# Performance work log

Hardware: AMD Instinct MI355X
Metric: run time of the kernel (lower is better)

## Reference

```python
import jax, jax.numpy as jnp
import numpy as np

INVALID = 1e9  # distance value marking a missing arc (>= 1e6 threshold in source)
TEMPERATURE = 0.5


def setup_inputs() -> dict:
    n = 4096
    key = jax.random.key(0)
    k_d, k_m, k_l = jax.random.split(key, 3)
    dist = jax.random.uniform(k_d, (n, n), dtype=jnp.float32, minval=0.0, maxval=100.0)
    keep = jax.random.uniform(k_m, (n, n)) < 0.5
    distance_matrix = jnp.where(keep, dist, INVALID).astype(jnp.float32)
    logits = (-2.0 + 0.5 * jax.random.normal(k_l, (n, n))).astype(jnp.float32)
    attention_logits = jnp.zeros((n, n), dtype=jnp.float32)
    return {
        "distance_matrix": distance_matrix,
        "logits": logits,
        "attention_logits": attention_logits,
        "source": 0,
        "destination": n - 1,
    }


def reference(distance_matrix, logits, attention_logits, source, destination):
    n = distance_matrix.shape[0]
    valid = (distance_matrix < 1e6).astype(jnp.float32)
    density = jnp.sum(valid) / (n * n)
    mu1 = 1.0
    mu2 = 10.0 * (1.0 + density)
    mu3 = 10.0 * (1.0 + density)

    # decision matrix (dense branch)
    attention = jax.nn.softmax(attention_logits, axis=1)
    x = jax.nn.sigmoid(logits / TEMPERATURE) * attention * valid  # [n, n]

    # flow penalty: vectorized form of the per-node loop
    out_flow = jnp.sum(x, axis=1)  # [n]
    in_flow = jnp.sum(x, axis=0)   # [n]
    d = out_flow - in_flow
    d = d.at[source].add(-1.0).at[destination].add(1.0)
    flow_penalty = jnp.sum(d * d)

    path_cost = jnp.sum(distance_matrix * x)  # invalid arcs have x == 0
    binary_penalty = jnp.sum(x * (1.0 - x))

    # connectivity: 10-step matmul power iteration (min(n-1, 10) = 10 for n > 11)
    reach = x
    for _ in range(10):
        reach = jnp.minimum(reach + reach @ x, 1.0)
    connectivity_penalty = jnp.square(1.0 - reach[source, destination])

    sparsity_penalty = jnp.sum(x) / (n * n)
    n_edges = jnp.sum(valid)

    return (mu1 * path_cost / (n_edges + 1e-6)
            + mu2 * flow_penalty / n
            + mu3 * binary_penalty / (n * n)
            + 20.0 * connectivity_penalty
            + 5.0 * sparsity_penalty)
```

## Files before the change

### kernel.cpp

```cpp
#include <hip/hip_runtime.h>
#include <hip/hip_bf16.h>
#include <cmath>

typedef unsigned short u16;
typedef unsigned int u32;

__device__ __forceinline__ float bf2f(u16 b) {
    return __uint_as_float(((u32)b) << 16);
}
__device__ __forceinline__ u16 f2bf(float f) {
    u32 u = __float_as_uint(f);
    u = (u + 0x7fffu + ((u >> 16) & 1u)) >> 16;
    return (u16)u;
}

__device__ __forceinline__ float wave_sum(float v) {
#pragma unroll
    for (int o = 32; o > 0; o >>= 1) v += __shfl_xor(v, o, 64);
    return v;
}

__device__ float block_sum(float v) {
    __shared__ float s[4];
    v = wave_sum(v);
    __syncthreads();
    if ((threadIdx.x & 63) == 0) s[threadIdx.x >> 6] = v;
    __syncthreads();
    return s[0] + s[1] + s[2] + s[3];
}

template <int NF4>
__global__ __launch_bounds__(256, 2) void k_main(
    const float* __restrict__ dist, const float* __restrict__ logit,
    const float* __restrict__ attn, const int* __restrict__ srcp,
    u16* __restrict__ xb, float* __restrict__ out_flow,
    float* __restrict__ cnt_row, float* __restrict__ s2_row,
    float* __restrict__ pc_row, float* __restrict__ v, int n) {
    const int lane = threadIdx.x & 63;
    const int wv = threadIdx.x >> 6;
    const int row = blockIdx.x * 4 + wv;
    const size_t base = (size_t)row * n;

    u32 apk[2 * NF4];
    float se = 0.f;
#pragma unroll
    for (int k = 0; k < NF4; ++k) {
        const float4 a = *(const float4*)(attn + base + 4 * lane + 256 * k);
        const float e0 = __expf(a.x), e1 = __expf(a.y);
        const float e2 = __expf(a.z), e3 = __expf(a.w);
        se += (e0 + e1) + (e2 + e3);
        apk[2 * k]     = ((u32)f2bf(e1) << 16) | (u32)f2bf(e0);
        apk[2 * k + 1] = ((u32)f2bf(e3) << 16) | (u32)f2bf(e2);
    }
    const float invZ = 1.0f / wave_sum(se);
    const int src = *srcp;

    float cnt = 0.f, s1 = 0.f, s2 = 0.f, pc = 0.f;
#pragma unroll
    for (int k = 0; k < NF4; ++k) {
        const int col = 4 * lane + 256 * k;
        const float4 df = *(const float4*)(dist + base + col);
        const float4 lf = *(const float4*)(logit + base + col);
        const float dv[4] = {df.x, df.y, df.z, df.w};
        const float lv[4] = {lf.x, lf.y, lf.z, lf.w};
        const float av[4] = {bf2f((u16)(apk[2 * k] & 0xffffu)),
                             bf2f((u16)(apk[2 * k] >> 16)),
                             bf2f((u16)(apk[2 * k + 1] & 0xffffu)),
                             bf2f((u16)(apk[2 * k + 1] >> 16))};
        float xv[4];
        ushort4 pk;
        u16* pkp = (u16*)&pk;
#pragma unroll
        for (int q = 0; q < 4; ++q) {
            float valid = (dv[q] < 1.0e6f) ? 1.f : 0.f;
            float sg = 1.0f / (1.0f + __expf(-2.0f * lv[q]));
            float x = sg * (av[q] * invZ) * valid;
            xv[q] = x;
            cnt += valid;
            s1 += x;
            s2 += x * x;
            pc += dv[q] * x;
            pkp[q] = f2bf(x);
        }
        *(ushort4*)(xb + base + col) = pk;
        if (row == src) {
            float4 vf; vf.x = xv[0]; vf.y = xv[1]; vf.z = xv[2]; vf.w = xv[3];
            *(float4*)(v + col) = vf;
        }
    }
#pragma unroll
    for (int o = 32; o > 0; o >>= 1) {
        cnt += __shfl_xor(cnt, o, 64);
        s1  += __shfl_xor(s1, o, 64);
        s2  += __shfl_xor(s2, o, 64);
        pc  += __shfl_xor(pc, o, 64);
    }
    if (lane == 0) {
        out_flow[row] = s1;
        cnt_row[row] = cnt;
        s2_row[row] = s2;
        pc_row[row] = pc;
    }
}

template <int FIRST>
__global__ __launch_bounds__(256) void k_iter(
    const u16* __restrict__ xb, const float* __restrict__ v_in,
    const float* __restrict__ up_in, float* __restrict__ v_out,
    float* __restrict__ up_out, float* __restrict__ ip,
    int n, int nbx, int rc) {
    __shared__ float vl[64];
    __shared__ float vparts[4][64];
    const int t = threadIdx.x;
    const int lin = blockIdx.x;
    const int xcd = lin & 7;
    const int slot = lin >> 3;
    const int bx = slot % nbx;
    const int by = xcd * ((gridDim.x >> 3) / nbx) + slot / nbx;
    const int rows_per = n / rc;
    const int i0 = by * rows_per;
    const int j0 = bx * 1024 + t * 4;

    if (FIRST) {
        if (t < rows_per) {
            float a = v_in[i0 + t];
            vl[t] = a;
            if (bx == 0) v_out[i0 + t] = a;
        }
    } else {
        const int i = t & 63, g = t >> 6;
        const int cpg = rc >> 2;
        float a = 0.f;
#pragma unroll 4
        for (int c = g * cpg; c < (g + 1) * cpg; ++c)
            a += up_in[(size_t)c * n + i0 + i];
        vparts[g][i] = a;
        __syncthreads();
        if (t < rows_per) {
            float s = v_in[i0 + t] + vparts[0][t] + vparts[1][t] +
                      vparts[2][t] + vparts[3][t];
            vl[t] = s;
            if (bx == 0) v_out[i0 + t] = s;
        }
    }
    __syncthreads();

    float4 acc = {0.f, 0.f, 0.f, 0.f};
    float4 cs = {0.f, 0.f, 0.f, 0.f};
#pragma unroll 8
    for (int i = 0; i < rows_per; ++i) {
        ushort4 xv = *(const ushort4*)(xb + (size_t)(i0 + i) * n + j0);
        float vi = vl[i];
        acc.x = fmaf(vi, bf2f(xv.x), acc.x);
        acc.y = fmaf(vi, bf2f(xv.y), acc.y);
        acc.z = fmaf(vi, bf2f(xv.z), acc.z);
        acc.w = fmaf(vi, bf2f(xv.w), acc.w);
        if (FIRST) {
            cs.x += bf2f(xv.x); cs.y += bf2f(xv.y);
            cs.z += bf2f(xv.z); cs.w += bf2f(xv.w);
        }
    }
    *(float4*)(up_out + (size_t)by * n + j0) = acc;
    if (FIRST) *(float4*)(ip + (size_t)by * n + j0) = cs;
}

__global__ __launch_bounds__(256) void k_reduce(
    const float* __restrict__ out_flow, const float* __restrict__ ip,
    const float* __restrict__ cnt_row, const float* __restrict__ s2_row,
    const float* __restrict__ pc_row, const int* __restrict__ srcp,
    const int* __restrict__ dstp, float* __restrict__ pb, int n, int nchunk) {
    const int t = threadIdx.x;
    const int j = blockIdx.x * 256 + t;
    const int src = *srcp, dst = *dstp;
    float infl = 0.f;
#pragma unroll 8
    for (int c = 0; c < nchunk; ++c) infl += ip[(size_t)c * n + j];
    float d = out_flow[j] - infl;
    if (j == src) d -= 1.f;
    if (j == dst) d += 1.f;
    float f = block_sum(d * d);
    float s1 = block_sum(out_flow[j]);
    float cnt = block_sum(cnt_row[j]);
    float s2 = block_sum(s2_row[j]);
    float pc = block_sum(pc_row[j]);
    if (t == 0) {
        float* p = pb + blockIdx.x * 5;
        p[0] = f; p[1] = s1; p[2] = cnt; p[3] = s2; p[4] = pc;
    }
}

__global__ __launch_bounds__(256) void k_final(
    const float* __restrict__ pb, const float* __restrict__ v_last,
    const float* __restrict__ up_last, const int* __restrict__ dstp,
    float* __restrict__ out, int n, int nblk, int nchunk) {
    const int t = threadIdx.x;
    const int dst = *dstp;
    float flow = block_sum(t < nblk ? pb[t * 5 + 0] : 0.f);
    float S1   = block_sum(t < nblk ? pb[t * 5 + 1] : 0.f);
    float NE   = block_sum(t < nblk ? pb[t * 5 + 2] : 0.f);
    float S2   = block_sum(t < nblk ? pb[t * 5 + 3] : 0.f);
    float PC   = block_sum(t < nblk ? pb[t * 5 + 4] : 0.f);
    float r = block_sum(t < nchunk ? up_last[(size_t)t * n + dst] : 0.f);
    if (t == 0) {
        r += v_last[dst];
        float nf = (float)n;
        float nn = nf * nf;
        float density = NE / nn;
        float mu2 = 10.f * (1.f + density);
        float om = 1.f - r;
        float res = PC / (NE + 1e-6f)
                  + mu2 * flow / nf
                  + mu2 * (S1 - S2) / nn
                  + 20.f * om * om
                  + 5.f * S1 / nn;
        out[0] = res;
    }
}

extern "C" void kernel_launch(void* const* d_in, const int* in_sizes, int n_in,
                              void* d_out, int out_size, void* d_ws, size_t ws_size,
                              hipStream_t stream) {
    const float* dist = (const float*)d_in[0];
    const float* logit = (const float*)d_in[1];
    const float* attn = (const float*)d_in[2];
    const int* srcp = (const int*)d_in[3];
    const int* dstp = (const int*)d_in[4];
    const int n = (int)(std::sqrt((double)in_sizes[0]) + 0.5);
    const size_t nn = (size_t)n * n;

    const int RC = 64;
    const int nbx = n / 1024;

    char* ws = (char*)d_ws;
    u16* xb = (u16*)ws;
    float* f = (float*)(ws + nn * sizeof(u16));
    float* out_flow = f; f += n;
    float* cnt_row = f;  f += n;
    float* s2_row = f;   f += n;
    float* pc_row = f;   f += n;
    float* vA = f;       f += n;
    float* vB = f;       f += n;
    float* upA = f;      f += (size_t)RC * n;
    float* upB = f;      f += (size_t)RC * n;
    float* ip = f;       f += (size_t)RC * n;
    float* pb = f;       f += 128;

    switch (n >> 8) {
        case 16: k_main<16><<<n / 4, 256, 0, stream>>>(dist, logit, attn, srcp,
                     xb, out_flow, cnt_row, s2_row, pc_row, vA, n); break;
        case 8:  k_main<8><<<n / 4, 256, 0, stream>>>(dist, logit, attn, srcp,
                     xb, out_flow, cnt_row, s2_row, pc_row, vA, n); break;
        case 4:  k_main<4><<<n / 4, 256, 0, stream>>>(dist, logit, attn, srcp,
                     xb, out_flow, cnt_row, s2_row, pc_row, vA, n); break;
        default: k_main<16><<<n / 4, 256, 0, stream>>>(dist, logit, attn, srcp,
                     xb, out_flow, cnt_row, s2_row, pc_row, vA, n); break;
    }

    const int niblk = nbx * RC;

    k_iter<1><<<niblk, 256, 0, stream>>>(xb, vA, nullptr, vB, upA, ip, n, nbx, RC);
    float* vin = vB;  float* uin = upA;
    float* vout;      float* uout;
    for (int it = 2; it <= 10; ++it) {
        vout = (it & 1) ? vB : vA;
        uout = (it & 1) ? upA : upB;
        k_iter<0><<<niblk, 256, 0, stream>>>(xb, vin, uin, vout, uout, nullptr,
                                             n, nbx, RC);
        vin = vout; uin = uout;
    }

    k_reduce<<<n / 256, 256, 0, stream>>>(out_flow, ip, cnt_row, s2_row,
                                          pc_row, srcp, dstp, pb, n, RC);
    k_final<<<1, 256, 0, stream>>>(pb, vin, uin, dstp, (float*)d_out, n,
                                   n / 256, RC);
}
```

Baseline: 117.5 us.

## Split row softmax denominator into separate kernel, one block per row

The fused per-wave kernel, which held a whole row's exp(attention) packed in registers, is replaced by two kernels. One computes each row's softmax denominator, and a second re-reads the attention row, recomputes exp, and builds x with block-level reductions. The aim is to cut register pressure and raise occupancy and memory parallelism in the x-building pass. In exchange it reads the attention matrix from HBM a second time (64 MB more traffic) and adds a kernel launch.

After: 124.8 us. 6.2% more time.

```diff
diff --git a/kernel.cpp b/kernel.cpp
--- a/kernel.cpp
+++ b/kernel.cpp
@@ -29,44 +29,45 @@
     return s[0] + s[1] + s[2] + s[3];
 }
 
-template <int NF4>
-__global__ __launch_bounds__(256, 2) void k_main(
+template <int K>
+__global__ __launch_bounds__(256) void k_denom(
+    const float* __restrict__ attn, float* __restrict__ Zrow, int n) {
+    const int row = blockIdx.x;
+    const int t = threadIdx.x;
+    const size_t base = (size_t)row * n;
+    float se = 0.f;
+#pragma unroll 2
+    for (int k = 0; k < K; ++k) {
+        const float4 a = *(const float4*)(attn + base + 4 * t + 1024 * k);
+        se += (__expf(a.x) + __expf(a.y)) + (__expf(a.z) + __expf(a.w));
+    }
+    se = block_sum(se);
+    if (t == 0) Zrow[row] = se;
+}
+
+template <int K>
+__global__ __launch_bounds__(256) void k_x(
     const float* __restrict__ dist, const float* __restrict__ logit,
-    const float* __restrict__ attn, const int* __restrict__ srcp,
-    u16* __restrict__ xb, float* __restrict__ out_flow,
-    float* __restrict__ cnt_row, float* __restrict__ s2_row,
-    float* __restrict__ pc_row, float* __restrict__ v, int n) {
-    const int lane = threadIdx.x & 63;
-    const int wv = threadIdx.x >> 6;
-    const int row = blockIdx.x * 4 + wv;
+    const float* __restrict__ attn, const float* __restrict__ Zrow,
+    const int* __restrict__ srcp, u16* __restrict__ xb,
+    float* __restrict__ out_flow, float* __restrict__ cnt_row,
+    float* __restrict__ s2_row, float* __restrict__ pc_row,
+    float* __restrict__ v, int n) {
+    const int row = blockIdx.x;
+    const int t = threadIdx.x;
     const size_t base = (size_t)row * n;
-
-    u32 apk[2 * NF4];
-    float se = 0.f;
-#pragma unroll
-    for (int k = 0; k < NF4; ++k) {
-        const float4 a = *(const float4*)(attn + base + 4 * lane + 256 * k);
-        const float e0 = __expf(a.x), e1 = __expf(a.y);
-        const float e2 = __expf(a.z), e3 = __expf(a.w);
-        se += (e0 + e1) + (e2 + e3);
-        apk[2 * k]     = ((u32)f2bf(e1) << 16) | (u32)f2bf(e0);
-        apk[2 * k + 1] = ((u32)f2bf(e3) << 16) | (u32)f2bf(e2);
-    }
-    const float invZ = 1.0f / wave_sum(se);
+    const float invZ = 1.0f / Zrow[row];
     const int src = *srcp;
-
     float cnt = 0.f, s1 = 0.f, s2 = 0.f, pc = 0.f;
-#pragma unroll
-    for (int k = 0; k < NF4; ++k) {
-        const int col = 4 * lane + 256 * k;
+#pragma unroll 2
+    for (int k = 0; k < K; ++k) {
+        const int col = 4 * t + 1024 * k;
+        const float4 af = *(const float4*)(attn + base + col);
         const float4 df = *(const float4*)(dist + base + col);
         const float4 lf = *(const float4*)(logit + base + col);
+        const float av[4] = {af.x, af.y, af.z, af.w};
         const float dv[4] = {df.x, df.y, df.z, df.w};
         const float lv[4] = {lf.x, lf.y, lf.z, lf.w};
-        const float av[4] = {bf2f((u16)(apk[2 * k] & 0xffffu)),
-                             bf2f((u16)(apk[2 * k] >> 16)),
-                             bf2f((u16)(apk[2 * k + 1] & 0xffffu)),
-                             bf2f((u16)(apk[2 * k + 1] >> 16))};
         float xv[4];
         ushort4 pk;
         u16* pkp = (u16*)&pk;
@@ -74,7 +75,7 @@
         for (int q = 0; q < 4; ++q) {
             float valid = (dv[q] < 1.0e6f) ? 1.f : 0.f;
             float sg = 1.0f / (1.0f + __expf(-2.0f * lv[q]));
-            float x = sg * (av[q] * invZ) * valid;
+            float x = sg * (__expf(av[q]) * invZ) * valid;
             xv[q] = x;
             cnt += valid;
             s1 += x;
@@ -88,14 +89,11 @@
             *(float4*)(v + col) = vf;
         }
     }
-#pragma unroll
-    for (int o = 32; o > 0; o >>= 1) {
-        cnt += __shfl_xor(cnt, o, 64);
-        s1  += __shfl_xor(s1, o, 64);
-        s2  += __shfl_xor(s2, o, 64);
-        pc  += __shfl_xor(pc, o, 64);
-    }
-    if (lane == 0) {
+    s1 = block_sum(s1);
+    cnt = block_sum(cnt);
+    s2 = block_sum(s2);
+    pc = block_sum(pc);
+    if (t == 0) {
         out_flow[row] = s1;
         cnt_row[row] = cnt;
         s2_row[row] = s2;
@@ -240,20 +238,33 @@
     float* pc_row = f;   f += n;
     float* vA = f;       f += n;
     float* vB = f;       f += n;
+    float* zrow = f;     f += n;
     float* upA = f;      f += (size_t)RC * n;
     float* upB = f;      f += (size_t)RC * n;
     float* ip = f;       f += (size_t)RC * n;
     float* pb = f;       f += 128;
 
-    switch (n >> 8) {
-        case 16: k_main<16><<<n / 4, 256, 0, stream>>>(dist, logit, attn, srcp,
-                     xb, out_flow, cnt_row, s2_row, pc_row, vA, n); break;
-        case 8:  k_main<8><<<n / 4, 256, 0, stream>>>(dist, logit, attn, srcp,
-                     xb, out_flow, cnt_row, s2_row, pc_row, vA, n); break;
-        case 4:  k_main<4><<<n / 4, 256, 0, stream>>>(dist, logit, attn, srcp,
-                     xb, out_flow, cnt_row, s2_row, pc_row, vA, n); break;
-        default: k_main<16><<<n / 4, 256, 0, stream>>>(dist, logit, attn, srcp,
-                     xb, out_flow, cnt_row, s2_row, pc_row, vA, n); break;
+    switch (n >> 10) {
+        case 4:
+            k_denom<4><<<n, 256, 0, stream>>>(attn, zrow, n);
+            k_x<4><<<n, 256, 0, stream>>>(dist, logit, attn, zrow, srcp, xb,
+                out_flow, cnt_row, s2_row, pc_row, vA, n);
+            break;
+        case 2:
+            k_denom<2><<<n, 256, 0, stream>>>(attn, zrow, n);
+            k_x<2><<<n, 256, 0, stream>>>(dist, logit, attn, zrow, srcp, xb,
+                out_flow, cnt_row, s2_row, pc_row, vA, n);
+            break;
+        case 8:
+            k_denom<8><<<n, 256, 0, stream>>>(attn, zrow, n);
+            k_x<8><<<n, 256, 0, stream>>>(dist, logit, attn, zrow, srcp, xb,
+                out_flow, cnt_row, s2_row, pc_row, vA, n);
+            break;
+        default:
+            k_denom<1><<<n, 256, 0, stream>>>(attn, zrow, n);
+            k_x<1><<<n, 256, 0, stream>>>(dist, logit, attn, zrow, srcp, xb,
+                out_flow, cnt_row, s2_row, pc_row, vA, n);
+            break;
     }
 
     const int niblk = nbx * RC;
```

## Process one row per block with upfront batched loads in x-construction kernel

Applied to the files above, without the earlier changes.

The elementwise decision-matrix kernel now assigns a whole row to a 256-thread block instead of one row per wave. All attention, distance and logit float4 loads are issued up front into registers, giving more memory parallelism, and the bf16 packing of exp(attention) is dropped in favour of keeping floats. Launch bounds rise to 4 blocks per SM, and the row reductions now go through block-wide shared-memory sums, which add barriers. A side effect is that the attention values are no longer rounded to bf16 before use.

After: 113.1 us. -3.8%, faster.

```diff
diff --git a/kernel.cpp b/kernel.cpp
--- a/kernel.cpp
+++ b/kernel.cpp
@@ -29,44 +29,45 @@
     return s[0] + s[1] + s[2] + s[3];
 }
 
-template <int NF4>
-__global__ __launch_bounds__(256, 2) void k_main(
+template <int K>
+__global__ __launch_bounds__(256, 4) void k_x(
     const float* __restrict__ dist, const float* __restrict__ logit,
     const float* __restrict__ attn, const int* __restrict__ srcp,
     u16* __restrict__ xb, float* __restrict__ out_flow,
     float* __restrict__ cnt_row, float* __restrict__ s2_row,
     float* __restrict__ pc_row, float* __restrict__ v, int n) {
-    const int lane = threadIdx.x & 63;
-    const int wv = threadIdx.x >> 6;
-    const int row = blockIdx.x * 4 + wv;
+    const int row = blockIdx.x;
+    const int t = threadIdx.x;
     const size_t base = (size_t)row * n;
 
-    u32 apk[2 * NF4];
+    float4 a4[K];
+#pragma unroll
+    for (int k = 0; k < K; ++k)
+        a4[k] = *(const float4*)(attn + base + 4 * t + 1024 * k);
     float se = 0.f;
 #pragma unroll
-    for (int k = 0; k < NF4; ++k) {
-        const float4 a = *(const float4*)(attn + base + 4 * lane + 256 * k);
-        const float e0 = __expf(a.x), e1 = __expf(a.y);
-        const float e2 = __expf(a.z), e3 = __expf(a.w);
-        se += (e0 + e1) + (e2 + e3);
-        apk[2 * k]     = ((u32)f2bf(e1) << 16) | (u32)f2bf(e0);
-        apk[2 * k + 1] = ((u32)f2bf(e3) << 16) | (u32)f2bf(e2);
-    }
-    const float invZ = 1.0f / wave_sum(se);
+    for (int k = 0; k < K; ++k) {
+        a4[k].x = __expf(a4[k].x); a4[k].y = __expf(a4[k].y);
+        a4[k].z = __expf(a4[k].z); a4[k].w = __expf(a4[k].w);
+        se += (a4[k].x + a4[k].y) + (a4[k].z + a4[k].w);
+    }
+    const float invZ = 1.0f / block_sum(se);
     const int src = *srcp;
 
+    float4 d4[K], l4[K];
+#pragma unroll
+    for (int k = 0; k < K; ++k) {
+        const int col = 4 * t + 1024 * k;
+        d4[k] = *(const float4*)(dist + base + col);
+        l4[k] = *(const float4*)(logit + base + col);
+    }
     float cnt = 0.f, s1 = 0.f, s2 = 0.f, pc = 0.f;
 #pragma unroll
-    for (int k = 0; k < NF4; ++k) {
-        const int col = 4 * lane + 256 * k;
-        const float4 df = *(const float4*)(dist + base + col);
-        const float4 lf = *(const float4*)(logit + base + col);
-        const float dv[4] = {df.x, df.y, df.z, df.w};
-        const float lv[4] = {lf.x, lf.y, lf.z, lf.w};
-        const float av[4] = {bf2f((u16)(apk[2 * k] & 0xffffu)),
-                             bf2f((u16)(apk[2 * k] >> 16)),
-                             bf2f((u16)(apk[2 * k + 1] & 0xffffu)),
-                             bf2f((u16)(apk[2 * k + 1] >> 16))};
+    for (int k = 0; k < K; ++k) {
+        const int col = 4 * t + 1024 * k;
+        const float av[4] = {a4[k].x, a4[k].y, a4[k].z, a4[k].w};
+        const float dv[4] = {d4[k].x, d4[k].y, d4[k].z, d4[k].w};
+        const float lv[4] = {l4[k].x, l4[k].y, l4[k].z, l4[k].w};
         float xv[4];
         ushort4 pk;
         u16* pkp = (u16*)&pk;
@@ -88,14 +89,11 @@
             *(float4*)(v + col) = vf;
         }
     }
-#pragma unroll
-    for (int o = 32; o > 0; o >>= 1) {
-        cnt += __shfl_xor(cnt, o, 64);
-        s1  += __shfl_xor(s1, o, 64);
-        s2  += __shfl_xor(s2, o, 64);
-        pc  += __shfl_xor(pc, o, 64);
-    }
-    if (lane == 0) {
+    s1 = block_sum(s1);
+    cnt = block_sum(cnt);
+    s2 = block_sum(s2);
+    pc = block_sum(pc);
+    if (t == 0) {
         out_flow[row] = s1;
         cnt_row[row] = cnt;
         s2_row[row] = s2;
@@ -245,15 +243,15 @@
     float* ip = f;       f += (size_t)RC * n;
     float* pb = f;       f += 128;
 
-    switch (n >> 8) {
-        case 16: k_main<16><<<n / 4, 256, 0, stream>>>(dist, logit, attn, srcp,
-                     xb, out_flow, cnt_row, s2_row, pc_row, vA, n); break;
-        case 8:  k_main<8><<<n / 4, 256, 0, stream>>>(dist, logit, attn, srcp,
-                     xb, out_flow, cnt_row, s2_row, pc_row, vA, n); break;
-        case 4:  k_main<4><<<n / 4, 256, 0, stream>>>(dist, logit, attn, srcp,
-                     xb, out_flow, cnt_row, s2_row, pc_row, vA, n); break;
-        default: k_main<16><<<n / 4, 256, 0, stream>>>(dist, logit, attn, srcp,
-                     xb, out_flow, cnt_row, s2_row, pc_row, vA, n); break;
+    switch (n >> 10) {
+        case 4: k_x<4><<<n, 256, 0, stream>>>(dist, logit, attn, srcp, xb,
+                    out_flow, cnt_row, s2_row, pc_row, vA, n); break;
+        case 2: k_x<2><<<n, 256, 0, stream>>>(dist, logit, attn, srcp, xb,
+                    out_flow, cnt_row, s2_row, pc_row, vA, n); break;
+        case 8: k_x<8><<<n, 256, 0, stream>>>(dist, logit, attn, srcp, xb,
+                    out_flow, cnt_row, s2_row, pc_row, vA, n); break;
+        default: k_x<1><<<n, 256, 0, stream>>>(dist, logit, attn, srcp, xb,
+                    out_flow, cnt_row, s2_row, pc_row, vA, n); break;
     }
 
     const int niblk = nbx * RC;
```
